# Kernel tuning notes

Hardware: AMD Instinct MI355X
Metric: run time of the kernel (lower is better)

The kernel has to match this reference:

```python
import jax, jax.numpy as jnp
import numpy as np
from jax import lax

VOCAB = 60      # len(ALL_CHARS): BOS + 52 letters + " .,;'-" + EOS
EMB = 100       # emb_dim
HID = 100       # HIDDEN_SIZE
SEQ = 262144    # long-document sequence length


def setup_inputs() -> dict:
    key = jax.random.key(0)
    k = jax.random.split(key, 6)
    s = 1.0 / np.sqrt(HID)  # PyTorch GRU init scale
    x = jax.random.randint(k[0], (1, SEQ), 0, VOCAB)
    emb = jax.random.normal(k[1], (VOCAB, EMB), dtype=jnp.float32)
    w_ih = jax.random.uniform(k[2], (3 * HID, EMB), minval=-s, maxval=s, dtype=jnp.float32)
    w_hh = jax.random.uniform(k[3], (3 * HID, HID), minval=-s, maxval=s, dtype=jnp.float32)
    b_ih = jax.random.uniform(k[4], (3 * HID,), minval=-s, maxval=s, dtype=jnp.float32)
    b_hh = jax.random.uniform(k[5], (3 * HID,), minval=-s, maxval=s, dtype=jnp.float32)
    return {"x": x, "emb": emb, "w_ih": w_ih, "w_hh": w_hh, "b_ih": b_ih, "b_hh": b_hh}


def reference(x, emb, w_ih, w_hh, b_ih, b_hh):
    # Embedding lookup: [1, S] -> [S, E]  (batch asserted == 1 in original)
    xe = emb[x[0]]
    # Precompute input-side gate projections for all timesteps: [S, 3H]
    xp = xe @ w_ih.T + b_ih
    H = w_hh.shape[1]
    w_hr, w_hz, w_hn = w_hh[:H], w_hh[H:2 * H], w_hh[2 * H:]
    b_hr, b_hz, b_hn = b_hh[:H], b_hh[H:2 * H], b_hh[2 * H:]

    def step(h, xp_t):
        xr, xz, xn = xp_t[:H], xp_t[H:2 * H], xp_t[2 * H:]
        r = jax.nn.sigmoid(xr + h @ w_hr.T + b_hr)
        z = jax.nn.sigmoid(xz + h @ w_hz.T + b_hz)
        n = jnp.tanh(xn + r * (h @ w_hn.T + b_hn))
        h_new = (1.0 - z) * n + z * h
        return h_new, None

    h0 = jnp.zeros((H,), dtype=xp.dtype)
    h_last, _ = lax.scan(step, h0, xp)
    # Match torch GRU h_n shape: [num_layers=1, batch=1, HID]
    return h_last[None, None, :]
```

## Files before the change

### kernel.cpp

```cpp
#include <hip/hip_runtime.h>
#include <stdint.h>

#define VOCAB 60
#define EMB   100
#define HID   100
#define SEQN  262144
#define NPROJ 300
#define KPAD  128
#define NMFW  4
#define MT    6
#define KS    4

typedef float    f32x4 __attribute__((ext_vector_type(4)));
typedef _Float16 h16x8 __attribute__((ext_vector_type(8)));

__device__ __forceinline__ float fast_sig(float x) {
    return __builtin_amdgcn_rcpf(1.0f + __builtin_amdgcn_exp2f(-1.442695041f * x));
}
__device__ __forceinline__ float fast_tanh(float x) {
    return 2.0f * __builtin_amdgcn_rcpf(1.0f + __builtin_amdgcn_exp2f(-2.885390082f * x)) - 1.0f;
}

__global__ void precompute_kernel(const float* __restrict__ emb,
                                  const float* __restrict__ w_ih,
                                  const float* __restrict__ b_ih,
                                  const float* __restrict__ b_hh,
                                  const float* __restrict__ w_hh,
                                  float* __restrict__ proj,
                                  _Float16* __restrict__ afrag)
{
    int idx = blockIdx.x * blockDim.x + threadIdx.x;
    if (idx < VOCAB * NPROJ) {
        int v = idx / NPROJ, j = idx - v * NPROJ;
        float acc = b_ih[j] + (j < 2 * HID ? b_hh[j] : 0.0f);
        const float* er = emb  + v * EMB;
        const float* wr = w_ih + j * EMB;
        #pragma unroll 4
        for (int k = 0; k < EMB; ++k) acc = fmaf(er[k], wr[k], acc);
        proj[idx] = acc;
    }
    if (idx < NMFW * MT * KS * 64 * 8) {
        int e    = idx & 7;
        int lane = (idx >> 3) & 63;
        int q0   = idx >> 9;
        int ks   = q0 & 3;
        int q1   = q0 >> 2;
        int m    = q1 % MT;
        int w    = q1 / MT;
        int rho  = lane & 15;
        int G    = rho >> 2, q = rho & 3;
        int wh   = m % 3;
        int j    = 32 * w + 8 * G + 2 * q + (m >= 3 ? 1 : 0);
        int k    = ks * 32 + ((lane >> 4) << 3) + e;
        afrag[idx] = (j < HID && k < HID)
                   ? (_Float16)w_hh[(wh * HID + j) * HID + k] : (_Float16)0.0f;
    }
}

#define MFMA(A, B, C) __builtin_amdgcn_mfma_f32_16x16x32_f16((A), (B), (C), 0, 0, 0)

#define LOADF(M, K) \
    h16x8 af_##M##_##K = *(const h16x8*)(afrag + ((((wave*MT+(M))*KS+(K))*64) + lane) * 8);

#define BAR() asm volatile("s_waitcnt lgkmcnt(0)\n\ts_barrier" ::: "memory")

#define B_LOAD(BUF) {                                   \
    const _Float16* hp_ = hbuf[BUF];                    \
    b0 = *(const h16x8*)(hp_ +  0 + ko);                \
    b1 = *(const h16x8*)(hp_ + 32 + ko);                \
    b2 = *(const h16x8*)(hp_ + 64 + ko);                \
    b3 = *(const h16x8*)(hp_ + 96 + ko); }

#define STEP(CUR, NXT, TOFF) {                                              \
          \
    asm("" : "+a"(af_0_0), "+a"(af_0_1), "+a"(af_0_2), "+a"(af_0_3), "+a"(af_1_0)); \
    asm("" : "+a"(af_1_1), "+a"(af_1_2), "+a"(af_1_3), "+a"(af_2_0), "+a"(af_2_1)); \
    asm("" : "+a"(af_2_2), "+a"(af_2_3), "+a"(af_3_0), "+a"(af_3_1), "+a"(af_3_2)); \
    asm("" : "+a"(af_3_3), "+a"(af_4_0), "+a"(af_4_1), "+a"(af_4_2), "+a"(af_4_3)); \
    asm("" : "+a"(af_5_0), "+a"(af_5_1), "+a"(af_5_2), "+a"(af_5_3));       \
         \
    int tt_ = t + (TOFF);                                                   \
    int tok_nn = x[(tt_ + 2 < SEQN) ? (tt_ + 2) : (SEQN - 1)];              \
    int tok_s  = __builtin_amdgcn_readfirstlane(tok_next);                  \
    const float* pb_ = projj + tok_s * NPROJ;                               \
    float xr_n = pb_[0];                                                    \
    float xz_n = pb_[HID];                                                  \
    float xn_n = pb_[2 * HID];                                              \
         \
    f32x4 zz = {0.f, 0.f, 0.f, 0.f};                                        \
    f32x4 ac0 = zz, ac1 = zz, ac2 = zz, ac3 = zz, ac4 = zz, ac5 = zz;       \
    ac0 = MFMA(af_0_0, b0, ac0); ac1 = MFMA(af_1_0, b0, ac1);               \
    ac2 = MFMA(af_2_0, b0, ac2); ac3 = MFMA(af_3_0, b0, ac3);               \
    ac4 = MFMA(af_4_0, b0, ac4); ac5 = MFMA(af_5_0, b0, ac5);               \
    ac0 = MFMA(af_0_1, b1, ac0); ac1 = MFMA(af_1_1, b1, ac1);               \
    ac2 = MFMA(af_2_1, b1, ac2); ac3 = MFMA(af_3_1, b1, ac3);               \
    ac4 = MFMA(af_4_1, b1, ac4); ac5 = MFMA(af_5_1, b1, ac5);               \
    ac0 = MFMA(af_0_2, b2, ac0); ac1 = MFMA(af_1_2, b2, ac1);               \
    ac2 = MFMA(af_2_2, b2, ac2); ac3 = MFMA(af_3_2, b2, ac3);               \
    ac4 = MFMA(af_4_2, b2, ac4); ac5 = MFMA(af_5_2, b2, ac5);               \
    ac0 = MFMA(af_0_3, b3, ac0); ac1 = MFMA(af_1_3, b3, ac1);               \
    ac2 = MFMA(af_2_3, b3, ac2); ac3 = MFMA(af_3_3, b3, ac3);               \
    ac4 = MFMA(af_4_3, b3, ac4); ac5 = MFMA(af_5_3, b3, ac5);               \
                                \
    f32x4 acR = hi ? ac3 : ac0;                                             \
    f32x4 acZ = hi ? ac4 : ac1;                                             \
    f32x4 acN = hi ? ac5 : ac2;                                             \
    float sRlo = (q2 & 1) ? acR[1] : acR[0], sRhi = (q2 & 1) ? acR[3] : acR[2]; \
    float sZlo = (q2 & 1) ? acZ[1] : acZ[0], sZhi = (q2 & 1) ? acZ[3] : acZ[2]; \
    float sNlo = (q2 & 1) ? acN[1] : acN[0], sNhi = (q2 & 1) ? acN[3] : acN[2]; \
    float sR = (q2 & 2) ? sRhi : sRlo;                                      \
    float sZ = (q2 & 2) ? sZhi : sZlo;                                      \
    float sN = (q2 & 2) ? sNhi : sNlo;                                      \
                                                            \
    float r    = fast_sig(sR + xr);                                         \
    float z    = fast_sig(sZ + xz);                                         \
    float n    = fast_tanh(xn + r * (sN + bhn));                            \
    float hnew = n + z * (hold - n);                                        \
    hold = hnew;                                                            \
    if (active) hbuf[NXT][j] = (_Float16)hnew;                              \
    BAR();                                                                  \
    B_LOAD(NXT);                    \
    tok_next = tok_nn;                                                      \
    xr = xr_n;  xz = xz_n;  xn = xn_n; }

__global__ __launch_bounds__(256, 1) __attribute__((amdgpu_waves_per_eu(1, 1)))
void gru_seq_kernel(const int*      __restrict__ x,
                    const float*    __restrict__ b_hh,
                    const float*    __restrict__ proj,
                    const _Float16* __restrict__ afrag,
                    float*          __restrict__ out)
{
    __shared__ __align__(16) _Float16 hbuf[2][KPAD];

    const int tid  = threadIdx.x;
    const int wave = tid >> 6;
    const int lane = tid & 63;
    const int G    = lane >> 4;
    const int c    = lane & 15;
    const int ko   = (lane >> 4) << 3;

    const int  jv     = 32 * wave + 8 * G + c;
    const bool active = (c < 8) && (jv < HID);
    const int  j      = active ? jv : 0;
    const int  q2     = (c >> 1) & 3;
    const bool hi     = (c & 1);

    if (tid < 2 * KPAD) ((_Float16*)hbuf)[tid] = (_Float16)0.0f;

    LOADF(0,0) LOADF(0,1) LOADF(0,2) LOADF(0,3)
    LOADF(1,0) LOADF(1,1) LOADF(1,2) LOADF(1,3)
    LOADF(2,0) LOADF(2,1) LOADF(2,2) LOADF(2,3)
    LOADF(3,0) LOADF(3,1) LOADF(3,2) LOADF(3,3)
    LOADF(4,0) LOADF(4,1) LOADF(4,2) LOADF(4,3)
    LOADF(5,0) LOADF(5,1) LOADF(5,2) LOADF(5,3)

    const float  bhn   = b_hh[2 * HID + j];
    const float* projj = proj + j;
    float hold = 0.0f;

    int tok0 = x[0];
    float xr = projj[tok0 * NPROJ];
    float xz = projj[tok0 * NPROJ + HID];
    float xn = projj[tok0 * NPROJ + 2 * HID];
    int tok_next = x[1];

    h16x8 b0, b1, b2, b3;
    __syncthreads();
    B_LOAD(0);

    for (int t = 0; t < SEQN; t += 2) {
        STEP(0, 1, 0)
        STEP(1, 0, 1)
    }

    if (active) out[j] = hold;
}

extern "C" void kernel_launch(void* const* d_in, const int* in_sizes, int n_in,
                              void* d_out, int out_size, void* d_ws, size_t ws_size,
                              hipStream_t stream)
{
    const int*   x    = (const int*)  d_in[0];
    const float* emb  = (const float*)d_in[1];
    const float* w_ih = (const float*)d_in[2];
    const float* w_hh = (const float*)d_in[3];
    const float* b_ih = (const float*)d_in[4];
    const float* b_hh = (const float*)d_in[5];
    float* out = (float*)d_out;

    float*    proj  = (float*)d_ws;
    _Float16* afrag = (_Float16*)(proj + VOCAB * NPROJ);

    const int total = NMFW * MT * KS * 64 * 8;
    precompute_kernel<<<(total + 255) / 256, 256, 0, stream>>>(
        emb, w_ih, b_ih, b_hh, w_hh, proj, afrag);
    gru_seq_kernel<<<1, 256, 0, stream>>>(x, b_hh, proj, afrag, out);
}
```

Baseline: 101.7 ms.

## Drop fourth MFMA K-slice and compute the 4-element tail with fdot2

Reduces the recurrent matvec from four 32-wide K-slices to three (covering k<96), and handles the remaining four hidden elements per row with packed-half dot products using per-thread register weights. This removes six MFMAs and one LDS load from the serial per-step critical path. The trade is extra VALU dot2 work and a broadcast LDS read of the tail, and the gate computations are interleaved so that r is ready earlier. It also reorders MFMA issue and starts from zero accumulators.

```diff
diff --git a/kernel.cpp b/kernel.cpp
--- a/kernel.cpp
+++ b/kernel.cpp
@@ -6,12 +6,14 @@
 #define HID   100
 #define SEQN  262144
 #define NPROJ 300
-#define KPAD  128
+#define HSTR  104
 #define NMFW  4
 #define MT    6
-#define KS    4
+#define KS    3
 
 typedef float    f32x4 __attribute__((ext_vector_type(4)));
+typedef _Float16 h16x2 __attribute__((ext_vector_type(2)));
+typedef _Float16 h16x4 __attribute__((ext_vector_type(4)));
 typedef _Float16 h16x8 __attribute__((ext_vector_type(8)));
 
 __device__ __forceinline__ float fast_sig(float x) {
@@ -20,6 +22,17 @@
 __device__ __forceinline__ float fast_tanh(float x) {
     return 2.0f * __builtin_amdgcn_rcpf(1.0f + __builtin_amdgcn_exp2f(-2.885390082f * x)) - 1.0f;
 }
+
+#if __has_builtin(__builtin_amdgcn_fdot2)
+#define DOT2(A, B, C) __builtin_amdgcn_fdot2((A), (B), (C), false)
+#else
+__device__ __forceinline__ float DOT2(h16x2 a, h16x2 b, float c) {
+    return fmaf((float)a.x, (float)b.x, fmaf((float)a.y, (float)b.y, c));
+}
+#endif
+
+#define AS2(U)    __builtin_bit_cast(h16x2, (U))
+#define SH2(V, I) __builtin_shufflevector((V), (V), (I), (I) + 1)
 
 __global__ void precompute_kernel(const float* __restrict__ emb,
                                   const float* __restrict__ w_ih,
@@ -27,7 +40,8 @@
                                   const float* __restrict__ b_hh,
                                   const float* __restrict__ w_hh,
                                   float* __restrict__ proj,
-                                  _Float16* __restrict__ afrag)
+                                  _Float16* __restrict__ afrag,
+                                  _Float16* __restrict__ wtail)
 {
     int idx = blockIdx.x * blockDim.x + threadIdx.x;
     if (idx < VOCAB * NPROJ) {
@@ -43,8 +57,8 @@
         int e    = idx & 7;
         int lane = (idx >> 3) & 63;
         int q0   = idx >> 9;
-        int ks   = q0 & 3;
-        int q1   = q0 >> 2;
+        int ks   = q0 % KS;
+        int q1   = q0 / KS;
         int m    = q1 % MT;
         int w    = q1 / MT;
         int rho  = lane & 15;
@@ -52,8 +66,13 @@
         int wh   = m % 3;
         int j    = 32 * w + 8 * G + 2 * q + (m >= 3 ? 1 : 0);
         int k    = ks * 32 + ((lane >> 4) << 3) + e;
-        afrag[idx] = (j < HID && k < HID)
+        afrag[idx] = (j < HID)
                    ? (_Float16)w_hh[(wh * HID + j) * HID + k] : (_Float16)0.0f;
+    }
+    if (idx < 3 * HID * 4) {
+        int e = idx & 3;
+        int row = idx >> 2;
+        wtail[idx] = (_Float16)w_hh[row * HID + 96 + e];
     }
 }
 
@@ -62,22 +81,23 @@
 #define LOADF(M, K) \
     h16x8 af_##M##_##K = *(const h16x8*)(afrag + ((((wave*MT+(M))*KS+(K))*64) + lane) * 8);
 
+#define PIN(D) asm("v_mov_b32 %0, %0" : "+v"(D));
+
 #define BAR() asm volatile("s_waitcnt lgkmcnt(0)\n\ts_barrier" ::: "memory")
 
 #define B_LOAD(BUF) {                                   \
     const _Float16* hp_ = hbuf[BUF];                    \
-    b0 = *(const h16x8*)(hp_ +  0 + ko);                \
-    b1 = *(const h16x8*)(hp_ + 32 + ko);                \
-    b2 = *(const h16x8*)(hp_ + 64 + ko);                \
-    b3 = *(const h16x8*)(hp_ + 96 + ko); }
+    b0  = *(const h16x8*)(hp_ +  0 + ko);               \
+    b1  = *(const h16x8*)(hp_ + 32 + ko);               \
+    b2  = *(const h16x8*)(hp_ + 64 + ko);               \
+    hb4 = *(const h16x4*)(hp_ + 96); }
 
 #define STEP(CUR, NXT, TOFF) {                                              \
           \
-    asm("" : "+a"(af_0_0), "+a"(af_0_1), "+a"(af_0_2), "+a"(af_0_3), "+a"(af_1_0)); \
-    asm("" : "+a"(af_1_1), "+a"(af_1_2), "+a"(af_1_3), "+a"(af_2_0), "+a"(af_2_1)); \
-    asm("" : "+a"(af_2_2), "+a"(af_2_3), "+a"(af_3_0), "+a"(af_3_1), "+a"(af_3_2)); \
-    asm("" : "+a"(af_3_3), "+a"(af_4_0), "+a"(af_4_1), "+a"(af_4_2), "+a"(af_4_3)); \
-    asm("" : "+a"(af_5_0), "+a"(af_5_1), "+a"(af_5_2), "+a"(af_5_3));       \
+    asm("" : "+a"(af_0_0), "+a"(af_0_1), "+a"(af_0_2), "+a"(af_1_0), "+a"(af_1_1)); \
+    asm("" : "+a"(af_1_2), "+a"(af_2_0), "+a"(af_2_1), "+a"(af_2_2), "+a"(af_3_0)); \
+    asm("" : "+a"(af_3_1), "+a"(af_3_2), "+a"(af_4_0), "+a"(af_4_1), "+a"(af_4_2)); \
+    asm("" : "+a"(af_5_0), "+a"(af_5_1), "+a"(af_5_2));                     \
          \
     int tt_ = t + (TOFF);                                                   \
     int tok_nn = x[(tt_ + 2 < SEQN) ? (tt_ + 2) : (SEQN - 1)];              \
@@ -86,35 +106,38 @@
     float xr_n = pb_[0];                                                    \
     float xz_n = pb_[HID];                                                  \
     float xn_n = pb_[2 * HID];                                              \
-         \
+                      \
     f32x4 zz = {0.f, 0.f, 0.f, 0.f};                                        \
-    f32x4 ac0 = zz, ac1 = zz, ac2 = zz, ac3 = zz, ac4 = zz, ac5 = zz;       \
-    ac0 = MFMA(af_0_0, b0, ac0); ac1 = MFMA(af_1_0, b0, ac1);               \
-    ac2 = MFMA(af_2_0, b0, ac2); ac3 = MFMA(af_3_0, b0, ac3);               \
-    ac4 = MFMA(af_4_0, b0, ac4); ac5 = MFMA(af_5_0, b0, ac5);               \
-    ac0 = MFMA(af_0_1, b1, ac0); ac1 = MFMA(af_1_1, b1, ac1);               \
-    ac2 = MFMA(af_2_1, b1, ac2); ac3 = MFMA(af_3_1, b1, ac3);               \
-    ac4 = MFMA(af_4_1, b1, ac4); ac5 = MFMA(af_5_1, b1, ac5);               \
-    ac0 = MFMA(af_0_2, b2, ac0); ac1 = MFMA(af_1_2, b2, ac1);               \
-    ac2 = MFMA(af_2_2, b2, ac2); ac3 = MFMA(af_3_2, b2, ac3);               \
-    ac4 = MFMA(af_4_2, b2, ac4); ac5 = MFMA(af_5_2, b2, ac5);               \
-    ac0 = MFMA(af_0_3, b3, ac0); ac1 = MFMA(af_1_3, b3, ac1);               \
-    ac2 = MFMA(af_2_3, b3, ac2); ac3 = MFMA(af_3_3, b3, ac3);               \
-    ac4 = MFMA(af_4_3, b3, ac4); ac5 = MFMA(af_5_3, b3, ac5);               \
-                                \
+    f32x4 ac0, ac1, ac2, ac3, ac4, ac5;                                     \
+    ac0 = MFMA(af_0_0, b0, zz);  ac3 = MFMA(af_3_0, b0, zz);                \
+    ac1 = MFMA(af_1_0, b0, zz);  ac4 = MFMA(af_4_0, b0, zz);                \
+    ac2 = MFMA(af_2_0, b0, zz);  ac5 = MFMA(af_5_0, b0, zz);                \
+    ac0 = MFMA(af_0_1, b1, ac0); ac3 = MFMA(af_3_1, b1, ac3);               \
+    ac1 = MFMA(af_1_1, b1, ac1); ac4 = MFMA(af_4_1, b1, ac4);               \
+    ac2 = MFMA(af_2_1, b1, ac2); ac5 = MFMA(af_5_1, b1, ac5);               \
+    ac0 = MFMA(af_0_2, b2, ac0); ac3 = MFMA(af_3_2, b2, ac3);               \
+    ac1 = MFMA(af_1_2, b2, ac1); ac4 = MFMA(af_4_2, b2, ac4);               \
+    ac2 = MFMA(af_2_2, b2, ac2); ac5 = MFMA(af_5_2, b2, ac5);               \
+                                                       \
+    h16x2 hb01 = SH2(hb4, 0), hb23 = SH2(hb4, 2);                           \
+                                 \
     f32x4 acR = hi ? ac3 : ac0;                                             \
+    float sRl = (q2 & 1) ? acR[1] : acR[0], sRh = (q2 & 1) ? acR[3] : acR[2]; \
+    float sR  = (q2 & 2) ? sRh : sRl;                                       \
+    float tR  = DOT2(AS2(wtR01), hb01, DOT2(AS2(wtR23), hb23, 0.0f));       \
+    float r   = fast_sig(sR + tR + xr);                                     \
+                                                                \
     f32x4 acZ = hi ? ac4 : ac1;                                             \
+    float sZl = (q2 & 1) ? acZ[1] : acZ[0], sZh = (q2 & 1) ? acZ[3] : acZ[2]; \
+    float sZ  = (q2 & 2) ? sZh : sZl;                                       \
+    float tZ  = DOT2(AS2(wtZ01), hb01, DOT2(AS2(wtZ23), hb23, 0.0f));       \
+    float z   = fast_sig(sZ + tZ + xz);                                     \
+                                                  \
     f32x4 acN = hi ? ac5 : ac2;                                             \
-    float sRlo = (q2 & 1) ? acR[1] : acR[0], sRhi = (q2 & 1) ? acR[3] : acR[2]; \
-    float sZlo = (q2 & 1) ? acZ[1] : acZ[0], sZhi = (q2 & 1) ? acZ[3] : acZ[2]; \
-    float sNlo = (q2 & 1) ? acN[1] : acN[0], sNhi = (q2 & 1) ? acN[3] : acN[2]; \
-    float sR = (q2 & 2) ? sRhi : sRlo;                                      \
-    float sZ = (q2 & 2) ? sZhi : sZlo;                                      \
-    float sN = (q2 & 2) ? sNhi : sNlo;                                      \
-                                                            \
-    float r    = fast_sig(sR + xr);                                         \
-    float z    = fast_sig(sZ + xz);                                         \
-    float n    = fast_tanh(xn + r * (sN + bhn));                            \
+    float sNl = (q2 & 1) ? acN[1] : acN[0], sNh = (q2 & 1) ? acN[3] : acN[2]; \
+    float sN  = (q2 & 2) ? sNh : sNl;                                       \
+    float tN  = DOT2(AS2(wtN01), hb01, DOT2(AS2(wtN23), hb23, 0.0f));       \
+    float n   = fast_tanh(xn + r * (sN + tN + bhn));                        \
     float hnew = n + z * (hold - n);                                        \
     hold = hnew;                                                            \
     if (active) hbuf[NXT][j] = (_Float16)hnew;                              \
@@ -128,9 +151,10 @@
                     const float*    __restrict__ b_hh,
                     const float*    __restrict__ proj,
                     const _Float16* __restrict__ afrag,
+                    const _Float16* __restrict__ wtail,
                     float*          __restrict__ out)
 {
-    __shared__ __align__(16) _Float16 hbuf[2][KPAD];
+    __shared__ __align__(16) _Float16 hbuf[2][HSTR];
 
     const int tid  = threadIdx.x;
     const int wave = tid >> 6;
@@ -145,14 +169,20 @@
     const int  q2     = (c >> 1) & 3;
     const bool hi     = (c & 1);
 
-    if (tid < 2 * KPAD) ((_Float16*)hbuf)[tid] = (_Float16)0.0f;
-
-    LOADF(0,0) LOADF(0,1) LOADF(0,2) LOADF(0,3)
-    LOADF(1,0) LOADF(1,1) LOADF(1,2) LOADF(1,3)
-    LOADF(2,0) LOADF(2,1) LOADF(2,2) LOADF(2,3)
-    LOADF(3,0) LOADF(3,1) LOADF(3,2) LOADF(3,3)
-    LOADF(4,0) LOADF(4,1) LOADF(4,2) LOADF(4,3)
-    LOADF(5,0) LOADF(5,1) LOADF(5,2) LOADF(5,3)
+    if (tid < 2 * HSTR) ((_Float16*)hbuf)[tid] = (_Float16)0.0f;
+
+    LOADF(0,0) LOADF(0,1) LOADF(0,2)
+    LOADF(1,0) LOADF(1,1) LOADF(1,2)
+    LOADF(2,0) LOADF(2,1) LOADF(2,2)
+    LOADF(3,0) LOADF(3,1) LOADF(3,2)
+    LOADF(4,0) LOADF(4,1) LOADF(4,2)
+    LOADF(5,0) LOADF(5,1) LOADF(5,2)
+
+    const uint32_t* wt32 = (const uint32_t*)wtail;
+    uint32_t wtR01 = wt32[(0 * HID + j) * 2],     wtR23 = wt32[(0 * HID + j) * 2 + 1];
+    uint32_t wtZ01 = wt32[(1 * HID + j) * 2],     wtZ23 = wt32[(1 * HID + j) * 2 + 1];
+    uint32_t wtN01 = wt32[(2 * HID + j) * 2],     wtN23 = wt32[(2 * HID + j) * 2 + 1];
+    PIN(wtR01) PIN(wtR23) PIN(wtZ01) PIN(wtZ23) PIN(wtN01) PIN(wtN23)
 
     const float  bhn   = b_hh[2 * HID + j];
     const float* projj = proj + j;
@@ -164,7 +194,8 @@
     float xn = projj[tok0 * NPROJ + 2 * HID];
     int tok_next = x[1];
 
-    h16x8 b0, b1, b2, b3;
+    h16x8 b0, b1, b2;
+    h16x4 hb4;
     __syncthreads();
     B_LOAD(0);
 
@@ -190,9 +221,10 @@
 
     float*    proj  = (float*)d_ws;
     _Float16* afrag = (_Float16*)(proj + VOCAB * NPROJ);
+    _Float16* wtail = afrag + NMFW * MT * KS * 64 * 8;
 
     const int total = NMFW * MT * KS * 64 * 8;
     precompute_kernel<<<(total + 255) / 256, 256, 0, stream>>>(
-        emb, w_ih, b_ih, b_hh, w_hh, proj, afrag);
-    gru_seq_kernel<<<1, 256, 0, stream>>>(x, b_hh, proj, afrag, out);
-}
+        emb, w_ih, b_ih, b_hh, w_hh, proj, afrag, wtail);
+    gru_seq_kernel<<<1, 256, 0, stream>>>(x, b_hh, proj, afrag, wtail, out);
+}
```

Measured after the change: 95.06 ms. -6.5%, faster.
